# Performance work log

Measured on AMD Instinct MI355X. Metric: run time of the kernel, lower is better.

The kernel has to match this reference:

```python
import jax, jax.numpy as jnp
import numpy as np

ALPHA = 0.2       # LeakyReLU negative slope
NEG_INF = -9e15   # matches torch's -9000000000000000.0 masking constant


def setup_inputs() -> dict:
    key = jax.random.key(0)
    k1, k2, k3, k4 = jax.random.split(key, 4)
    N, Cin, T, V = 16, 64, 512, 64   # in_channels == out_channels == V == C (forced by module math)
    x = jax.random.normal(k1, (N, Cin, T, V), dtype=jnp.float32)
    # K=3 adjacency partitions with 0/1 entries; forward sums over dim 0 and masks where sum > 0
    A = jax.random.randint(k2, (3, V, V), 0, 2).astype(jnp.float32)
    # learned params (xavier-ish scale)
    W = jax.random.normal(k3, (V, V), dtype=jnp.float32) * 0.15
    a = jax.random.normal(k4, (2 * Cin, 1), dtype=jnp.float32) * 0.15
    return {"x": x, "A": A, "W": W, "a": a}


def reference(x, A, W, a):
    # x: [N, C, T, V_in]; W contracts the vertex dim (last axis), as in torch.matmul(x, W)
    x = jnp.einsum('nctv,vu->nctu', x, W)
    N, C, T, V = x.shape
    xf = x.transpose(0, 2, 3, 1).reshape(N * T, V, C)   # [B, V, C], B = N*T
    Asum = jnp.sum(A, axis=0)                           # [V, V]
    # e[b,i,j] = leakyrelu(cat(x_i, x_j) @ a) = leakyrelu(x_i@a1 + x_j@a2)
    a1, a2 = a[:C, 0], a[C:, 0]                         # [C], [C]
    f = xf @ a1                                         # [B, V]
    g = xf @ a2                                         # [B, V]
    e = jax.nn.leaky_relu(f[:, :, None] + g[:, None, :], ALPHA)  # [B, V, V]
    att = jnp.where(Asum[None, :, :] > 0, e, NEG_INF)
    att = jax.nn.softmax(att, axis=2)
    # dropout is identity in eval mode
    out = jnp.einsum('bij,bjc->bic', att, xf)           # [B, V, C]
    return out.reshape(N, T, V, C).transpose(0, 3, 1, 2)  # [N, C, T, V]
```

## Files before the change

kernel.cpp:

```cpp
#include <hip/hip_runtime.h>
#include <hip/hip_bf16.h>


using bf16x8 = __attribute__((ext_vector_type(8))) short;
using f32x4  = __attribute__((ext_vector_type(4))) float;
typedef unsigned long long ull;

constexpr float ALPHA = 0.2f;
constexpr float LOG2E = 1.4426950408889634f;

__device__ __forceinline__ unsigned short f2bf(float f) {
    union { __hip_bfloat16 h; unsigned short s; } u;
    u.h = __float2bfloat16(f);
    return u.s;
}

__global__ void prep_kernel(const float* __restrict__ A,
                            const float* __restrict__ W,
                            unsigned short* __restrict__ Wt,
                            ull* __restrict__ mask) {
    const int tid = threadIdx.x;
    const int v = tid & 63, q = tid >> 6;
    #pragma unroll 4
    for (int m = 0; m < 16; ++m) {
        const int u = 16 * q + m;
        Wt[v * 64 + u] = f2bf(W[u * 64 + v]);
    }
    if (tid < 64) {
        ull m = 0;
        for (int j = 0; j < 64; ++j) {
            float s = A[tid * 64 + j] + A[4096 + tid * 64 + j] + A[8192 + tid * 64 + j];
            if (s > 0.f) m |= (1ull << j);
        }
        mask[tid] = m;
    }
}

__global__ __launch_bounds__(256, 8) void gat_kernel(
    const float* __restrict__ x,
    const float* __restrict__ a,
    const unsigned short* __restrict__ Wt,
    const ull* __restrict__ maskbits,
    float* __restrict__ out)
{
    __shared__ unsigned short XbYb[64 * 72];
    __shared__ unsigned short WtPb[64 * 72];
    __shared__ float fpart[4][64];
    __shared__ float gpart[4][64];

    const int tid = threadIdx.x;
    const int b = blockIdx.x;
    const int n = b >> 9, t = b & 511;
    const int w = tid >> 6, lane = tid & 63;
    const int fr = lane & 15, hi = lane >> 4;
    const int fk = hi * 8;

    {
        const int c = tid >> 2, q = tid & 3;
        const float* xp = x + (size_t)n * 2097152 + (size_t)c * 32768
                            + (size_t)t * 64 + q * 16;
        float4 v0 = ((const float4*)xp)[0];
        float4 v1 = ((const float4*)xp)[1];
        float4 v2 = ((const float4*)xp)[2];
        float4 v3 = ((const float4*)xp)[3];
        union { bf16x8 v; unsigned short s[8]; } u0, u1;
        u0.s[0]=f2bf(v0.x); u0.s[1]=f2bf(v0.y); u0.s[2]=f2bf(v0.z); u0.s[3]=f2bf(v0.w);
        u0.s[4]=f2bf(v1.x); u0.s[5]=f2bf(v1.y); u0.s[6]=f2bf(v1.z); u0.s[7]=f2bf(v1.w);
        u1.s[0]=f2bf(v2.x); u1.s[1]=f2bf(v2.y); u1.s[2]=f2bf(v2.z); u1.s[3]=f2bf(v2.w);
        u1.s[4]=f2bf(v3.x); u1.s[5]=f2bf(v3.y); u1.s[6]=f2bf(v3.z); u1.s[7]=f2bf(v3.w);
        *(bf16x8*)&XbYb[c * 72 + q * 16]     = u0.v;
        *(bf16x8*)&XbYb[c * 72 + q * 16 + 8] = u1.v;
    }
    #pragma unroll
    for (int p = 0; p < 2; ++p) {
        const int r  = (tid >> 3) + 32 * p;
        const int cc = (tid & 7) * 8;
        *(bf16x8*)&WtPb[r * 72 + cc] = *(const bf16x8*)&Wt[r * 64 + cc];
    }
    __syncthreads();

    {
        f32x4 acc[4] = {{0,0,0,0},{0,0,0,0},{0,0,0,0},{0,0,0,0}};
        #pragma unroll
        for (int kc = 0; kc < 2; ++kc) {
            bf16x8 af = *(const bf16x8*)&XbYb[(16 * w + fr) * 72 + 32 * kc + fk];
            #pragma unroll
            for (int cb = 0; cb < 4; ++cb) {
                bf16x8 bfr = *(const bf16x8*)&WtPb[(16 * cb + fr) * 72 + 32 * kc + fk];
                acc[cb] = __builtin_amdgcn_mfma_f32_16x16x32_bf16(af, bfr, acc[cb], 0, 0, 0);
            }
        }
        const float4 a1v = *(const float4*)&a[16 * w + 4 * hi];
        const float4 a2v = *(const float4*)&a[64 + 16 * w + 4 * hi];
        #pragma unroll
        for (int cb = 0; cb < 4; ++cb) {
            #pragma unroll
            for (int r = 0; r < 4; ++r)
                XbYb[(16 * w + 4 * hi + r) * 72 + 16 * cb + fr] = f2bf(acc[cb][r]);
            float F = acc[cb][0]*a1v.x + acc[cb][1]*a1v.y + acc[cb][2]*a1v.z + acc[cb][3]*a1v.w;
            float G = acc[cb][0]*a2v.x + acc[cb][1]*a2v.y + acc[cb][2]*a2v.z + acc[cb][3]*a2v.w;
            F += __shfl_xor(F, 16, 64); F += __shfl_xor(F, 32, 64);
            G += __shfl_xor(G, 16, 64); G += __shfl_xor(G, 32, 64);
            if (lane < 16) {
                fpart[w][16 * cb + lane] = F * LOG2E;
                gpart[w][16 * cb + lane] = G * LOG2E;
            }
        }
    }
    __syncthreads();

    {
        const float gj = (gpart[0][lane] + gpart[1][lane]) + (gpart[2][lane] + gpart[3][lane]);
        #pragma unroll 4
        for (int k = 0; k < 16; ++k) {
            const int i = 16 * w + k;
            const ull mi = maskbits[i];
            const float fi = (fpart[0][i] + fpart[1][i]) + (fpart[2][i] + fpart[3][i]);
            const float s0 = fi + gj;
            const float e = fmaxf(s0, ALPHA * s0);
            const float p = (mi == 0ull) ? 1.0f
                          : (((mi >> lane) & 1ull) ? exp2f(e) : 0.0f);
            WtPb[i * 72 + lane] = f2bf(p);
        }
    }
    __syncthreads();

    {
        union { bf16x8 v; unsigned short s[8]; } ones;
        #pragma unroll
        for (int j = 0; j < 8; ++j) ones.s[j] = 0x3f80;
        bf16x8 pb0 = *(const bf16x8*)&WtPb[(16 * w + fr) * 72 + fk];
        bf16x8 pb1 = *(const bf16x8*)&WtPb[(16 * w + fr) * 72 + 32 + fk];
        f32x4 accS = {0, 0, 0, 0};
        accS = __builtin_amdgcn_mfma_f32_16x16x32_bf16(ones.v, pb0, accS, 0, 0, 0);
        accS = __builtin_amdgcn_mfma_f32_16x16x32_bf16(ones.v, pb1, accS, 0, 0, 0);
        f32x4 acc2[4] = {{0,0,0,0},{0,0,0,0},{0,0,0,0},{0,0,0,0}};
        #pragma unroll
        for (int rb = 0; rb < 4; ++rb) {
            bf16x8 y0 = *(const bf16x8*)&XbYb[(16 * rb + fr) * 72 + fk];
            bf16x8 y1 = *(const bf16x8*)&XbYb[(16 * rb + fr) * 72 + 32 + fk];
            acc2[rb] = __builtin_amdgcn_mfma_f32_16x16x32_bf16(y0, pb0, acc2[rb], 0, 0, 0);
            acc2[rb] = __builtin_amdgcn_mfma_f32_16x16x32_bf16(y1, pb1, acc2[rb], 0, 0, 0);
        }
        const float rs = __builtin_amdgcn_rcpf(accS[0]);
        float* op = out + (size_t)n * 2097152 + (size_t)t * 64 + 16 * w + fr;
        #pragma unroll
        for (int rb = 0; rb < 4; ++rb)
            #pragma unroll
            for (int r = 0; r < 4; ++r)
                op[(size_t)(16 * rb + 4 * hi + r) * 32768] = acc2[rb][r] * rs;
    }
}

extern "C" void kernel_launch(void* const* d_in, const int* in_sizes, int n_in,
                              void* d_out, int out_size, void* d_ws, size_t ws_size,
                              hipStream_t stream) {
    const float* x = (const float*)d_in[0];
    const float* A = (const float*)d_in[1];
    const float* W = (const float*)d_in[2];
    const float* a = (const float*)d_in[3];
    float* out = (float*)d_out;
    unsigned short* Wt = (unsigned short*)d_ws;
    ull* mask = (ull*)((char*)d_ws + 8192);

    prep_kernel<<<1, 256, 0, stream>>>(A, W, Wt, mask);
    gat_kernel<<<16 * 512, 256, 0, stream>>>(x, a, Wt, mask, out);
}
```

Measured before the change: 62.42 us.

## Make GAT kernel persistent with register prefetch of next tile's x

The kernel becomes persistent: a grid of 1536 blocks loops over the 8192 (n,t) tiles with a grid stride. While the current tile computes, each block prefetches the next tile's x slice into registers. W^T, the mask bits and the attention vector are loaded once per block, with the mask kept in shared memory. The row assignment in the softmax stage is interleaved across warps, and launch bounds drop to 6 blocks per CU. This trades per-block launch and reload overhead against fewer resident waves, an extra barrier per iteration, and register pressure from the prefetch.

Result: slower. 98.23 us (+57.4%).

```diff
diff --git a/kernel.cpp b/kernel.cpp
--- a/kernel.cpp
+++ b/kernel.cpp
@@ -8,6 +8,8 @@
 
 constexpr float ALPHA = 0.2f;
 constexpr float LOG2E = 1.4426950408889634f;
+constexpr int NB   = 8192;
+constexpr int GRID = 1536;
 
 __device__ __forceinline__ unsigned short f2bf(float f) {
     union { __hip_bfloat16 h; unsigned short s; } u;
@@ -20,10 +22,10 @@
                             unsigned short* __restrict__ Wt,
                             ull* __restrict__ mask) {
     const int tid = threadIdx.x;
-    const int v = tid & 63, q = tid >> 6;
+    const int v = tid & 63, qq = tid >> 6;
     #pragma unroll 4
     for (int m = 0; m < 16; ++m) {
-        const int u = 16 * q + m;
+        const int u = 16 * qq + m;
         Wt[v * 64 + u] = f2bf(W[u * 64 + v]);
     }
     if (tid < 64) {
@@ -36,7 +38,7 @@
     }
 }
 
-__global__ __launch_bounds__(256, 8) void gat_kernel(
+__global__ __launch_bounds__(256, 6) void gat_kernel(
     const float* __restrict__ x,
     const float* __restrict__ a,
     const unsigned short* __restrict__ Wt,
@@ -47,108 +49,134 @@
     __shared__ unsigned short WtPb[64 * 72];
     __shared__ float fpart[4][64];
     __shared__ float gpart[4][64];
+    __shared__ ull ml[64];
 
     const int tid = threadIdx.x;
-    const int b = blockIdx.x;
-    const int n = b >> 9, t = b & 511;
     const int w = tid >> 6, lane = tid & 63;
-    const int fr = lane & 15, hi = lane >> 4;
-    const int fk = hi * 8;
+    const int fr = lane & 15, hi = lane >> 4, fk = hi * 8;
+    const int c = tid >> 2, q = tid & 3;
 
+    if (tid < 64) ml[tid] = maskbits[tid];
+    const float4 a1v = *(const float4*)&a[16 * w + 4 * hi];
+    const float4 a2v = *(const float4*)&a[64 + 16 * w + 4 * hi];
+
+    const int wr = tid >> 3;
+    const int wc = (tid & 7) * 8;
+    bf16x8 wtr0 = *(const bf16x8*)&Wt[wr * 64 + wc];
+    bf16x8 wtr1 = *(const bf16x8*)&Wt[(wr + 32) * 64 + wc];
+
+    int b = blockIdx.x;
+    const size_t xoff = (size_t)c * 32768 + q * 16;
     {
-        const int c = tid >> 2, q = tid & 3;
-        const float* xp = x + (size_t)n * 2097152 + (size_t)c * 32768
-                            + (size_t)t * 64 + q * 16;
-        float4 v0 = ((const float4*)xp)[0];
-        float4 v1 = ((const float4*)xp)[1];
-        float4 v2 = ((const float4*)xp)[2];
-        float4 v3 = ((const float4*)xp)[3];
-        union { bf16x8 v; unsigned short s[8]; } u0, u1;
-        u0.s[0]=f2bf(v0.x); u0.s[1]=f2bf(v0.y); u0.s[2]=f2bf(v0.z); u0.s[3]=f2bf(v0.w);
-        u0.s[4]=f2bf(v1.x); u0.s[5]=f2bf(v1.y); u0.s[6]=f2bf(v1.z); u0.s[7]=f2bf(v1.w);
-        u1.s[0]=f2bf(v2.x); u1.s[1]=f2bf(v2.y); u1.s[2]=f2bf(v2.z); u1.s[3]=f2bf(v2.w);
-        u1.s[4]=f2bf(v3.x); u1.s[5]=f2bf(v3.y); u1.s[6]=f2bf(v3.z); u1.s[7]=f2bf(v3.w);
-        *(bf16x8*)&XbYb[c * 72 + q * 16]     = u0.v;
-        *(bf16x8*)&XbYb[c * 72 + q * 16 + 8] = u1.v;
-    }
-    #pragma unroll
-    for (int p = 0; p < 2; ++p) {
-        const int r  = (tid >> 3) + 32 * p;
-        const int cc = (tid & 7) * 8;
-        *(bf16x8*)&WtPb[r * 72 + cc] = *(const bf16x8*)&Wt[r * 64 + cc];
-    }
-    __syncthreads();
+        const float* xp = x + (size_t)(b >> 9) * 2097152 + (size_t)(b & 511) * 64 + xoff;
+        float4 xv0 = ((const float4*)xp)[0];
+        float4 xv1 = ((const float4*)xp)[1];
+        float4 xv2 = ((const float4*)xp)[2];
+        float4 xv3 = ((const float4*)xp)[3];
 
-    {
-        f32x4 acc[4] = {{0,0,0,0},{0,0,0,0},{0,0,0,0},{0,0,0,0}};
-        #pragma unroll
-        for (int kc = 0; kc < 2; ++kc) {
-            bf16x8 af = *(const bf16x8*)&XbYb[(16 * w + fr) * 72 + 32 * kc + fk];
-            #pragma unroll
-            for (int cb = 0; cb < 4; ++cb) {
-                bf16x8 bfr = *(const bf16x8*)&WtPb[(16 * cb + fr) * 72 + 32 * kc + fk];
-                acc[cb] = __builtin_amdgcn_mfma_f32_16x16x32_bf16(af, bfr, acc[cb], 0, 0, 0);
+        while (true) {
+            {
+                union { bf16x8 v; unsigned short s[8]; } u0, u1;
+                u0.s[0]=f2bf(xv0.x); u0.s[1]=f2bf(xv0.y); u0.s[2]=f2bf(xv0.z); u0.s[3]=f2bf(xv0.w);
+                u0.s[4]=f2bf(xv1.x); u0.s[5]=f2bf(xv1.y); u0.s[6]=f2bf(xv1.z); u0.s[7]=f2bf(xv1.w);
+                u1.s[0]=f2bf(xv2.x); u1.s[1]=f2bf(xv2.y); u1.s[2]=f2bf(xv2.z); u1.s[3]=f2bf(xv2.w);
+                u1.s[4]=f2bf(xv3.x); u1.s[5]=f2bf(xv3.y); u1.s[6]=f2bf(xv3.z); u1.s[7]=f2bf(xv3.w);
+                *(bf16x8*)&XbYb[c * 72 + q * 16]     = u0.v;
+                *(bf16x8*)&XbYb[c * 72 + q * 16 + 8] = u1.v;
+                *(bf16x8*)&WtPb[wr * 72 + wc]        = wtr0;
+                *(bf16x8*)&WtPb[(wr + 32) * 72 + wc] = wtr1;
             }
+            __syncthreads();
+
+            const int bn = b + GRID;
+            const bool last = (bn >= NB);
+            {
+                const int bl = last ? b : bn;
+                const float* xpn = x + (size_t)(bl >> 9) * 2097152
+                                     + (size_t)(bl & 511) * 64 + xoff;
+                xv0 = ((const float4*)xpn)[0];
+                xv1 = ((const float4*)xpn)[1];
+                xv2 = ((const float4*)xpn)[2];
+                xv3 = ((const float4*)xpn)[3];
+            }
+
+            {
+                f32x4 acc[4] = {{0,0,0,0},{0,0,0,0},{0,0,0,0},{0,0,0,0}};
+                #pragma unroll
+                for (int kc = 0; kc < 2; ++kc) {
+                    bf16x8 af = *(const bf16x8*)&XbYb[(16 * w + fr) * 72 + 32 * kc + fk];
+                    #pragma unroll
+                    for (int cb = 0; cb < 4; ++cb) {
+                        bf16x8 bfr = *(const bf16x8*)&WtPb[(16 * cb + fr) * 72 + 32 * kc + fk];
+                        acc[cb] = __builtin_amdgcn_mfma_f32_16x16x32_bf16(af, bfr, acc[cb], 0, 0, 0);
+                    }
+                }
+                #pragma unroll
+                for (int cb = 0; cb < 4; ++cb) {
+                    #pragma unroll
+                    for (int r = 0; r < 4; ++r)
+                        XbYb[(16 * w + 4 * hi + r) * 72 + 16 * cb + fr] = f2bf(acc[cb][r]);
+                    float F = acc[cb][0]*a1v.x + acc[cb][1]*a1v.y + acc[cb][2]*a1v.z + acc[cb][3]*a1v.w;
+                    float G = acc[cb][0]*a2v.x + acc[cb][1]*a2v.y + acc[cb][2]*a2v.z + acc[cb][3]*a2v.w;
+                    F += __shfl_xor(F, 16, 64); F += __shfl_xor(F, 32, 64);
+                    G += __shfl_xor(G, 16, 64); G += __shfl_xor(G, 32, 64);
+                    if (lane < 16) {
+                        fpart[w][16 * cb + lane] = F * LOG2E;
+                        gpart[w][16 * cb + lane] = G * LOG2E;
+                    }
+                }
+            }
+            __syncthreads();
+
+            {
+                const float gj = (gpart[0][lane] + gpart[1][lane])
+                               + (gpart[2][lane] + gpart[3][lane]);
+                #pragma unroll 4
+                for (int k = 0; k < 16; ++k) {
+                    const int i = 4 * k + w;
+                    const ull mi = ml[i];
+                    const float fi = (fpart[0][i] + fpart[1][i])
+                                   + (fpart[2][i] + fpart[3][i]);
+                    const float s0 = fi + gj;
+                    const float e = fmaxf(s0, ALPHA * s0);
+                    const float p = (mi == 0ull) ? 1.0f
+                                  : (((mi >> lane) & 1ull) ? exp2f(e) : 0.0f);
+                    WtPb[i * 72 + lane] = f2bf(p);
+                }
+            }
+            __syncthreads();
+
+            {
+                union { bf16x8 v; unsigned short s[8]; } ones;
+                #pragma unroll
+                for (int j = 0; j < 8; ++j) ones.s[j] = 0x3f80;
+                bf16x8 pb0 = *(const bf16x8*)&WtPb[(16 * w + fr) * 72 + fk];
+                bf16x8 pb1 = *(const bf16x8*)&WtPb[(16 * w + fr) * 72 + 32 + fk];
+                f32x4 accS = {0, 0, 0, 0};
+                accS = __builtin_amdgcn_mfma_f32_16x16x32_bf16(ones.v, pb0, accS, 0, 0, 0);
+                accS = __builtin_amdgcn_mfma_f32_16x16x32_bf16(ones.v, pb1, accS, 0, 0, 0);
+                f32x4 acc2[4] = {{0,0,0,0},{0,0,0,0},{0,0,0,0},{0,0,0,0}};
+                #pragma unroll
+                for (int rb = 0; rb < 4; ++rb) {
+                    bf16x8 y0 = *(const bf16x8*)&XbYb[(16 * rb + fr) * 72 + fk];
+                    bf16x8 y1 = *(const bf16x8*)&XbYb[(16 * rb + fr) * 72 + 32 + fk];
+                    acc2[rb] = __builtin_amdgcn_mfma_f32_16x16x32_bf16(y0, pb0, acc2[rb], 0, 0, 0);
+                    acc2[rb] = __builtin_amdgcn_mfma_f32_16x16x32_bf16(y1, pb1, acc2[rb], 0, 0, 0);
+                }
+                const float rs = __builtin_amdgcn_rcpf(accS[0]);
+                float* op = out + (size_t)(b >> 9) * 2097152 + (size_t)(b & 511) * 64
+                                + 16 * w + fr;
+                #pragma unroll
+                for (int rb = 0; rb < 4; ++rb)
+                    #pragma unroll
+                    for (int r = 0; r < 4; ++r)
+                        op[(size_t)(16 * rb + 4 * hi + r) * 32768] = acc2[rb][r] * rs;
+            }
+            __syncthreads();
+
+            if (last) break;
+            b = bn;
         }
-        const float4 a1v = *(const float4*)&a[16 * w + 4 * hi];
-        const float4 a2v = *(const float4*)&a[64 + 16 * w + 4 * hi];
-        #pragma unroll
-        for (int cb = 0; cb < 4; ++cb) {
-            #pragma unroll
-            for (int r = 0; r < 4; ++r)
-                XbYb[(16 * w + 4 * hi + r) * 72 + 16 * cb + fr] = f2bf(acc[cb][r]);
-            float F = acc[cb][0]*a1v.x + acc[cb][1]*a1v.y + acc[cb][2]*a1v.z + acc[cb][3]*a1v.w;
-            float G = acc[cb][0]*a2v.x + acc[cb][1]*a2v.y + acc[cb][2]*a2v.z + acc[cb][3]*a2v.w;
-            F += __shfl_xor(F, 16, 64); F += __shfl_xor(F, 32, 64);
-            G += __shfl_xor(G, 16, 64); G += __shfl_xor(G, 32, 64);
-            if (lane < 16) {
-                fpart[w][16 * cb + lane] = F * LOG2E;
-                gpart[w][16 * cb + lane] = G * LOG2E;
-            }
-        }
-    }
-    __syncthreads();
-
-    {
-        const float gj = (gpart[0][lane] + gpart[1][lane]) + (gpart[2][lane] + gpart[3][lane]);
-        #pragma unroll 4
-        for (int k = 0; k < 16; ++k) {
-            const int i = 16 * w + k;
-            const ull mi = maskbits[i];
-            const float fi = (fpart[0][i] + fpart[1][i]) + (fpart[2][i] + fpart[3][i]);
-            const float s0 = fi + gj;
-            const float e = fmaxf(s0, ALPHA * s0);
-            const float p = (mi == 0ull) ? 1.0f
-                          : (((mi >> lane) & 1ull) ? exp2f(e) : 0.0f);
-            WtPb[i * 72 + lane] = f2bf(p);
-        }
-    }
-    __syncthreads();
-
-    {
-        union { bf16x8 v; unsigned short s[8]; } ones;
-        #pragma unroll
-        for (int j = 0; j < 8; ++j) ones.s[j] = 0x3f80;
-        bf16x8 pb0 = *(const bf16x8*)&WtPb[(16 * w + fr) * 72 + fk];
-        bf16x8 pb1 = *(const bf16x8*)&WtPb[(16 * w + fr) * 72 + 32 + fk];
-        f32x4 accS = {0, 0, 0, 0};
-        accS = __builtin_amdgcn_mfma_f32_16x16x32_bf16(ones.v, pb0, accS, 0, 0, 0);
-        accS = __builtin_amdgcn_mfma_f32_16x16x32_bf16(ones.v, pb1, accS, 0, 0, 0);
-        f32x4 acc2[4] = {{0,0,0,0},{0,0,0,0},{0,0,0,0},{0,0,0,0}};
-        #pragma unroll
-        for (int rb = 0; rb < 4; ++rb) {
-            bf16x8 y0 = *(const bf16x8*)&XbYb[(16 * rb + fr) * 72 + fk];
-            bf16x8 y1 = *(const bf16x8*)&XbYb[(16 * rb + fr) * 72 + 32 + fk];
-            acc2[rb] = __builtin_amdgcn_mfma_f32_16x16x32_bf16(y0, pb0, acc2[rb], 0, 0, 0);
-            acc2[rb] = __builtin_amdgcn_mfma_f32_16x16x32_bf16(y1, pb1, acc2[rb], 0, 0, 0);
-        }
-        const float rs = __builtin_amdgcn_rcpf(accS[0]);
-        float* op = out + (size_t)n * 2097152 + (size_t)t * 64 + 16 * w + fr;
-        #pragma unroll
-        for (int rb = 0; rb < 4; ++rb)
-            #pragma unroll
-            for (int r = 0; r < 4; ++r)
-                op[(size_t)(16 * rb + 4 * hi + r) * 32768] = acc2[rb][r] * rs;
     }
 }
 
@@ -164,5 +192,5 @@
     ull* mask = (ull*)((char*)d_ws + 8192);
 
     prep_kernel<<<1, 256, 0, stream>>>(A, W, Wt, mask);
-    gat_kernel<<<16 * 512, 256, 0, stream>>>(x, a, Wt, mask, out);
+    gat_kernel<<<GRID, 256, 0, stream>>>(x, a, Wt, mask, out);
 }
```
